# Optimization experiments

Measured on AMD Instinct MI355X. Metric: run time of the kernel, lower is better.

The kernel has to match this reference:

```python
import jax, jax.numpy as jnp
import numpy as np

EPS = 1e-5        # torch BatchNorm2d default eps
G = 8             # DCNv4 groups
KP = 9            # 3x3 kernel points


def conv2d(x, w):
    return jax.lax.conv_general_dilated(
        x, w, window_strides=(1, 1), padding='SAME',
        dimension_numbers=('NCHW', 'OIHW', 'NCHW'))


def bn_eval(x, g_, b_, m_, v_):
    s = g_ / jnp.sqrt(v_ + EPS)
    return x * s[None, :, None, None] + (b_ - m_ * s)[None, :, None, None]


def silu(x):
    return x * jax.nn.sigmoid(x)


def dcnv4_core(value, offset, mask):
    # value: (N,H,W,G,Cg)  offset: (N,H,W,G,K,2) (x,y)  mask: (N,H,W,G,K) unnormalized (DCNv4: no softmax)
    N, H, W, Gn, Cg = value.shape
    r = jnp.arange(-1, 2, dtype=value.dtype)              # dilation=1, pad=1, 3x3 grid
    gy, gx = jnp.meshgrid(r, r, indexing='ij')
    grid_x = gx.ravel()  # (9,)
    grid_y = gy.ravel()
    px = jnp.arange(W, dtype=value.dtype)[None, None, :, None, None] + grid_x + offset[..., 0]
    py = jnp.arange(H, dtype=value.dtype)[None, :, None, None, None] + grid_y + offset[..., 1]
    x0 = jnp.floor(px); y0 = jnp.floor(py)
    lx = px - x0; ly = py - y0
    x0i = x0.astype(jnp.int32); y0i = y0.astype(jnp.int32)
    bidx = jnp.arange(N)[:, None, None, None, None]
    gidx = jnp.arange(Gn)[None, None, None, :, None]

    def tap(yi, xi, wgt):
        valid = (yi >= 0) & (yi < H) & (xi >= 0) & (xi < W)   # zero padding outside
        v = value[bidx, jnp.clip(yi, 0, H - 1), jnp.clip(xi, 0, W - 1), gidx]  # (N,H,W,G,K,Cg)
        return v * (wgt * valid)[..., None]

    s = (tap(y0i, x0i, (1 - ly) * (1 - lx))
         + tap(y0i, x0i + 1, (1 - ly) * lx)
         + tap(y0i + 1, x0i, ly * (1 - lx))
         + tap(y0i + 1, x0i + 1, ly * lx))
    return jnp.einsum('nhwgkc,nhwgk->nhwgc', s, mask)


def dcnv4(x, val_w, val_b, om_w, om_b, outp_w, outp_b):
    # x: NCHW. DCNv4 wrapper: flatten to tokens, value_proj, offset_mask linear on raw tokens,
    # deformable aggregation, output_proj, back to NCHW.
    N, C, H, W = x.shape
    t = x.transpose(0, 2, 3, 1).reshape(N, H * W, C)
    value = (t @ val_w.T + val_b).reshape(N, H, W, G, C // G)
    om = (t @ om_w.T + om_b).reshape(N, H, W, G, KP * 3)  # per group: 2K offsets then K masks
    offset = om[..., :2 * KP].reshape(N, H, W, G, KP, 2)
    mask = om[..., 2 * KP:]
    out = dcnv4_core(value, offset, mask).reshape(N, H * W, C)
    out = out @ outp_w.T + outp_b
    return out.reshape(N, H, W, C).transpose(0, 3, 1, 2)


def setup_inputs() -> dict:
    key = jax.random.key(0)
    ks = jax.random.split(key, 32)
    W_SC = 0.05
    d = {}
    d['x'] = jax.random.normal(ks[0], (4, 256, 64, 64), jnp.float32)
    d['cv1_w'] = jax.random.normal(ks[1], (128, 256, 3, 3), jnp.float32) * W_SC
    d['cv1_bn_g'] = jax.random.uniform(ks[2], (128,), jnp.float32, 0.5, 1.5)
    d['cv1_bn_b'] = jax.random.normal(ks[3], (128,), jnp.float32) * 0.1
    d['cv1_bn_m'] = jax.random.normal(ks[4], (128,), jnp.float32) * 0.1
    d['cv1_bn_v'] = jax.random.uniform(ks[5], (128,), jnp.float32, 0.5, 1.5)
    d['cv2_w'] = jax.random.normal(ks[6], (256, 128, 3, 3), jnp.float32) * W_SC
    d['cv2_bn_g'] = jax.random.uniform(ks[7], (256,), jnp.float32, 0.5, 1.5)
    d['cv2_bn_b'] = jax.random.normal(ks[8], (256,), jnp.float32) * 0.1
    d['cv2_bn_m'] = jax.random.normal(ks[9], (256,), jnp.float32) * 0.1
    d['cv2_bn_v'] = jax.random.uniform(ks[10], (256,), jnp.float32, 0.5, 1.5)
    d['val_w'] = jax.random.normal(ks[11], (256, 256), jnp.float32) * W_SC
    d['val_b'] = jax.random.normal(ks[12], (256,), jnp.float32) * 0.01
    d['om_w'] = jax.random.normal(ks[13], (216, 256), jnp.float32) * 0.02
    d['om_b'] = jax.random.normal(ks[14], (216,), jnp.float32) * 0.01
    d['outp_w'] = jax.random.normal(ks[15], (256, 256), jnp.float32) * W_SC
    d['outp_b'] = jax.random.normal(ks[16], (256,), jnp.float32) * 0.01
    d['bn3_g'] = jax.random.uniform(ks[17], (256,), jnp.float32, 0.5, 1.5)
    d['bn3_b'] = jax.random.normal(ks[18], (256,), jnp.float32) * 0.1
    d['bn3_m'] = jax.random.normal(ks[19], (256,), jnp.float32) * 0.1
    d['bn3_v'] = jax.random.uniform(ks[20], (256,), jnp.float32, 0.5, 1.5)
    d['pw1_w'] = jax.random.normal(ks[21], (768, 256, 1, 1), jnp.float32) * W_SC
    d['pw1_b'] = jax.random.normal(ks[22], (768,), jnp.float32) * 0.01
    d['pw2_w'] = jax.random.normal(ks[23], (256, 768, 1, 1), jnp.float32) * W_SC
    d['pw2_b'] = jax.random.normal(ks[24], (256,), jnp.float32) * 0.01
    return d


def reference(x, cv1_w, cv1_bn_g, cv1_bn_b, cv1_bn_m, cv1_bn_v,
              cv2_w, cv2_bn_g, cv2_bn_b, cv2_bn_m, cv2_bn_v,
              val_w, val_b, om_w, om_b, outp_w, outp_b,
              bn3_g, bn3_b, bn3_m, bn3_v, pw1_w, pw1_b, pw2_w, pw2_b):
    # cv2(cv1(x)) branch: Conv = Conv2d(no bias) + BN + SiLU
    y = silu(bn_eval(conv2d(x, cv1_w), cv1_bn_g, cv1_bn_b, cv1_bn_m, cv1_bn_v))
    y = silu(bn_eval(conv2d(y, cv2_w), cv2_bn_g, cv2_bn_b, cv2_bn_m, cv2_bn_v))
    # dcn branch: DCNv4 -> BN -> 1x1 conv (+SiLU) -> 1x1 conv
    d = dcnv4(x, val_w, val_b, om_w, om_b, outp_w, outp_b)
    d = bn_eval(d, bn3_g, bn3_b, bn3_m, bn3_v)
    d = silu(conv2d(d, pw1_w) + pw1_b[None, :, None, None])
    d = conv2d(d, pw2_w) + pw2_b[None, :, None, None]
    return x + y + d
```

## Files before the change

### kernel.cpp

```cpp
#include <hip/hip_runtime.h>
#include <math.h>

typedef __attribute__((ext_vector_type(8))) __bf16 bf16x8;
typedef __attribute__((ext_vector_type(8))) unsigned short us8;
typedef __attribute__((ext_vector_type(4))) unsigned short us4;
typedef __attribute__((ext_vector_type(4))) float f32x4;
typedef __attribute__((ext_vector_type(4))) int i32x4;
typedef unsigned int uint32;

#define EPSV 1e-5f

__device__ __forceinline__ float silu_f(float v) { return v / (1.f + __expf(-v)); }

__device__ __forceinline__ unsigned short f2bf(float f) {
  uint32 u = __builtin_bit_cast(uint32, f);
  u += 0x7fffu + ((u >> 16) & 1u);
  return (unsigned short)(u >> 16);
}
__device__ __forceinline__ float bf2f(unsigned short h) {
  uint32 u = ((uint32)h) << 16;
  return __builtin_bit_cast(float, u);
}

__device__ __forceinline__ void gl_lds16(const void* g, void* l) {
  __builtin_amdgcn_global_load_lds(
      (const __attribute__((address_space(1))) unsigned int*)g,
      (__attribute__((address_space(3))) unsigned int*)l, 16, 0, 0);
}

template <int EPI, int CIN, int BN>
__device__ __forceinline__ void gemm_body(
    int rb, int cb, int k0, int KL,
    const unsigned short* __restrict__ A, const unsigned short* __restrict__ Bw,
    const float* __restrict__ bias, int K, int Co, void* __restrict__ outv,
    const float* __restrict__ e0, const float* __restrict__ e1,
    const float* __restrict__ e2, const float* __restrict__ e3,
    const unsigned short* __restrict__ zpage, bf16x8* smem) {
  constexpr int NFR = BN / 32;
  constexpr int NB = BN / 64;
  constexpr int CPB = 512 + BN * 4;
  const int t = threadIdx.x;
  const int lane = t & 63;
  const int wv = t >> 6;
  const int wr = wv >> 1, wc = wv & 1;

  f32x4 acc[4][NFR];
#pragma unroll
  for (int i = 0; i < 4; i++)
#pragma unroll
    for (int j = 0; j < NFR; j++) acc[i][j] = (f32x4){0.f, 0.f, 0.f, 0.f};

  const unsigned short* Abase[2];
  int aprow[2], apcol[2], akoff[2];
#pragma unroll
  for (int i = 0; i < 2; i++) {
    int c = t + 256 * i;
    int row = (c >> 6) * 16 + (c & 15);
    int koff = ((c >> 4) & 3) * 8;
    akoff[i] = koff;
    int grow = rb + row;
    if constexpr (CIN > 0) {
      int n = grow >> 12, p = grow & 4095;
      aprow[i] = p >> 6;
      apcol[i] = p & 63;
      Abase[i] = A + (size_t)n * 4096 * CIN;
    } else {
      Abase[i] = A + (size_t)grow * K + koff;
    }
  }
  const unsigned short* Bbase[NB];
#pragma unroll
  for (int i = 0; i < NB; i++) {
    int c = t + 256 * i;
    int col = cb + (c >> 6) * 16 + (c & 15);
    int koff = ((c >> 4) & 3) * 8;
    Bbase[i] = (col < Co) ? (Bw + (size_t)col * K + koff) : zpage;
  }
  auto addrA = [&](int i, int kb) -> const unsigned short* {
    if constexpr (CIN > 0) {
      int tap = kb / CIN;
      int ci = (kb & (CIN - 1)) + akoff[i];
      int dy = tap / 3 - 1, dx = tap % 3 - 1;
      int h = aprow[i] + dy, w = apcol[i] + dx;
      if (((unsigned)h < 64u) & ((unsigned)w < 64u))
        return &Abase[i][(size_t)(h * 64 + w) * CIN + ci];
      return zpage;
    } else {
      return Abase[i] + kb;
    }
  };
  auto stage = [&](int buf, int kb) {
    bf16x8* base = &smem[buf * CPB];
    gl_lds16(addrA(0, kb), (void*)&base[t]);
    gl_lds16(addrA(1, kb), (void*)&base[t + 256]);
    gl_lds16((Bbase[0] == zpage) ? zpage : Bbase[0] + kb, (void*)&base[512 + t]);
    if constexpr (NB == 2)
      gl_lds16((Bbase[1] == zpage) ? zpage : Bbase[1] + kb,
               (void*)&base[512 + t + 256]);
  };

  const int nt = KL >> 5;
  stage(0, k0);
  __syncthreads();
  int cur = 0;
  for (int it = 0; it < nt; ++it) {
    if (it + 1 < nt) stage(cur ^ 1, k0 + ((it + 1) << 5));
    const bf16x8* Ab = &smem[cur * CPB];
    const bf16x8* Bb = Ab + 512;
    bf16x8 af[4], bfr[NFR];
#pragma unroll
    for (int mi = 0; mi < 4; mi++) af[mi] = Ab[(wr * 4 + mi) * 64 + lane];
#pragma unroll
    for (int ni = 0; ni < NFR; ni++) bfr[ni] = Bb[(wc * NFR + ni) * 64 + lane];
    __builtin_amdgcn_s_setprio(1);
#pragma unroll
    for (int mi = 0; mi < 4; mi++)
#pragma unroll
      for (int ni = 0; ni < NFR; ni++)
        acc[mi][ni] = __builtin_amdgcn_mfma_f32_16x16x32_bf16(af[mi], bfr[ni],
                                                              acc[mi][ni], 0, 0, 0);
    __builtin_amdgcn_s_setprio(0);
    __syncthreads();
    cur ^= 1;
  }

  const int lr = lane & 15, kg4 = (lane >> 4) * 4;
#pragma unroll
  for (int mi = 0; mi < 4; mi++) {
#pragma unroll
    for (int ni = 0; ni < NFR; ni++) {
      int gcol = cb + wc * (BN / 2) + ni * 16 + lr;
      if (gcol >= Co) continue;
      float bval, s = 1.f, tt = 0.f;
      if (EPI == 2 || EPI == 7) bval = 0.f;
      else if (EPI == 5) bval = (gcol < 256) ? bias[gcol] : e0[gcol - 256];
      else bval = bias[gcol];
      if (EPI == 2 || EPI == 3) {
        s = e0[gcol] * rsqrtf(e3[gcol] + EPSV);
        tt = e1[gcol] - e2[gcol] * s;
      }
      if (EPI == 6) {
        int grow0 = rb + wr * 64 + mi * 16 + kg4;
        int n = grow0 >> 12, p0 = grow0 & 4095;
        size_t oix = ((size_t)(n * 256 + gcol)) * 4096 + p0;
        f32x4 xv = *(const f32x4*)&((const float*)e0)[oix];
        const unsigned short* y2p = (const unsigned short*)e1;
        f32x4 ov;
#pragma unroll
        for (int j = 0; j < 4; j++) {
          float y2 = bf2f(y2p[((size_t)(n * 4096 + p0 + j)) * 256 + gcol]);
          ov[j] = acc[mi][ni][j] + bval + xv[j] + y2;
        }
        *(f32x4*)&((float*)outv)[oix] = ov;
        continue;
      }
#pragma unroll
      for (int j = 0; j < 4; j++) {
        int grow = rb + wr * 64 + mi * 16 + kg4 + j;
        float v = acc[mi][ni][j] + bval;
        if (EPI == 2) v = silu_f(v * s + tt);
        if (EPI == 3) v = v * s + tt;
        if (EPI == 4) v = silu_f(v);
        if (EPI == 5) {
          if (gcol < 256)
            ((unsigned short*)outv)[(size_t)grow * 256 + gcol] = f2bf(v);
          else
            ((unsigned short*)e1)[(size_t)grow * 216 + (gcol - 256)] = f2bf(v);
        } else {
          ((unsigned short*)outv)[(size_t)grow * Co + gcol] = f2bf(v);
        }
      }
    }
  }
}

template <int EPI, int CIN>
__device__ __forceinline__ void gemm_body64(
    int rb, int cb, int k0, int KL,
    const unsigned short* __restrict__ A, const unsigned short* __restrict__ Bw,
    const float* __restrict__ bias, int K, int Co, void* __restrict__ outv,
    const float* __restrict__ e0, const float* __restrict__ e1,
    const float* __restrict__ e2, const float* __restrict__ e3,
    const unsigned short* __restrict__ zpage, bf16x8* smem) {
  constexpr int CPB = 1536;
  const int t = threadIdx.x;
  const int lane = t & 63;
  const int wv = t >> 6;
  const int wr = wv >> 1, wc = wv & 1;

  f32x4 acc[4][2];
#pragma unroll
  for (int i = 0; i < 4; i++)
#pragma unroll
    for (int j = 0; j < 2; j++) acc[i][j] = (f32x4){0.f, 0.f, 0.f, 0.f};

  const unsigned short* Abase[4];
  int aprow[4], apcol[4], akoff[4];
#pragma unroll
  for (int i = 0; i < 4; i++) {
    int c = t + 256 * i;
    int row = (c >> 7) * 16 + (c & 15);
    int koff = ((c >> 6) & 1) * 32 + ((c >> 4) & 3) * 8;
    akoff[i] = koff;
    int grow = rb + row;
    if constexpr (CIN > 0) {
      int n = grow >> 12, p = grow & 4095;
      aprow[i] = p >> 6;
      apcol[i] = p & 63;
      Abase[i] = A + (size_t)n * 4096 * CIN;
    } else {
      Abase[i] = A + (size_t)grow * K + koff;
    }
  }
  const unsigned short* Bbase[2];
#pragma unroll
  for (int i = 0; i < 2; i++) {
    int c = t + 256 * i;
    int col = cb + (c >> 7) * 16 + (c & 15);
    int koff = ((c >> 6) & 1) * 32 + ((c >> 4) & 3) * 8;
    Bbase[i] = (col < Co) ? (Bw + (size_t)col * K + koff) : zpage;
  }
  auto addrA = [&](int i, int kb) -> const unsigned short* {
    if constexpr (CIN > 0) {
      int tap = kb / CIN;
      int ci = (kb & (CIN - 1)) + akoff[i];
      int dy = tap / 3 - 1, dx = tap % 3 - 1;
      int h = aprow[i] + dy, w = apcol[i] + dx;
      if (((unsigned)h < 64u) & ((unsigned)w < 64u))
        return &Abase[i][(size_t)(h * 64 + w) * CIN + ci];
      return zpage;
    } else {
      return Abase[i] + kb;
    }
  };
  auto stage = [&](int buf, int kb) {
    bf16x8* base = &smem[buf * CPB];
#pragma unroll
    for (int i = 0; i < 4; i++)
      gl_lds16(addrA(i, kb), (void*)&base[t + 256 * i]);
    gl_lds16((Bbase[0] == zpage) ? zpage : Bbase[0] + kb,
             (void*)&base[1024 + t]);
    gl_lds16((Bbase[1] == zpage) ? zpage : Bbase[1] + kb,
             (void*)&base[1024 + t + 256]);
  };

  const int nt = KL >> 6;
  stage(0, k0);
  __syncthreads();
  int cur = 0;
  for (int it = 0; it < nt; ++it) {
    if (it + 1 < nt) stage(cur ^ 1, k0 + ((it + 1) << 6));
    const bf16x8* Ab = &smem[cur * CPB];
    const bf16x8* Bb = Ab + 1024;
    __builtin_amdgcn_s_setprio(1);
#pragma unroll
    for (int ks = 0; ks < 2; ks++) {
      bf16x8 af[4], bfr[2];
#pragma unroll
      for (int mi = 0; mi < 4; mi++)
        af[mi] = Ab[((wr * 4 + mi) * 2 + ks) * 64 + lane];
#pragma unroll
      for (int ni = 0; ni < 2; ni++)
        bfr[ni] = Bb[((wc * 2 + ni) * 2 + ks) * 64 + lane];
#pragma unroll
      for (int mi = 0; mi < 4; mi++)
#pragma unroll
        for (int ni = 0; ni < 2; ni++)
          acc[mi][ni] = __builtin_amdgcn_mfma_f32_16x16x32_bf16(
              af[mi], bfr[ni], acc[mi][ni], 0, 0, 0);
    }
    __builtin_amdgcn_s_setprio(0);
    __syncthreads();
    cur ^= 1;
  }

  const int lr = lane & 15, kg4 = (lane >> 4) * 4;
#pragma unroll
  for (int mi = 0; mi < 4; mi++) {
#pragma unroll
    for (int ni = 0; ni < 2; ni++) {
      int gcol = cb + wc * 32 + ni * 16 + lr;
      if (gcol >= Co) continue;
      float bval, s = 1.f, tt = 0.f;
      if (EPI == 2) bval = 0.f;
      else bval = bias[gcol];
      if (EPI == 2 || EPI == 3) {
        s = e0[gcol] * rsqrtf(e3[gcol] + EPSV);
        tt = e1[gcol] - e2[gcol] * s;
      }
      if (EPI == 6) {
        int grow0 = rb + wr * 64 + mi * 16 + kg4;
        int n = grow0 >> 12, p0 = grow0 & 4095;
        size_t oix = ((size_t)(n * 256 + gcol)) * 4096 + p0;
        f32x4 xv = *(const f32x4*)&((const float*)e0)[oix];
        const unsigned short* y2p = (const unsigned short*)e1;
        f32x4 ov;
#pragma unroll
        for (int j = 0; j < 4; j++) {
          float y2 = bf2f(y2p[((size_t)(n * 4096 + p0 + j)) * 256 + gcol]);
          ov[j] = acc[mi][ni][j] + bval + xv[j] + y2;
        }
        *(f32x4*)&((float*)outv)[oix] = ov;
        continue;
      }
#pragma unroll
      for (int j = 0; j < 4; j++) {
        int grow = rb + wr * 64 + mi * 16 + kg4 + j;
        float v = acc[mi][ni][j] + bval;
        if (EPI == 2) v = silu_f(v * s + tt);
        if (EPI == 3) v = v * s + tt;
        ((unsigned short*)outv)[(size_t)grow * Co + gcol] = f2bf(v);
      }
    }
  }
}

__device__ __forceinline__ void dcn_body(
    int bid, const unsigned short* __restrict__ value,
    const unsigned short* __restrict__ om, unsigned short* __restrict__ out,
    void* smemraw) {
  f32x4* wgt = (f32x4*)smemraw;
  i32x4* adr = (i32x4*)((char*)smemraw + 576 * 16);
  const int n = bid >> 9;
  const int p0 = (bid & 511) * 8;
  const int t = threadIdx.x;

  for (int idx = t; idx < 576; idx += 256) {
    int pi = idx / 72;
    int gk = idx - pi * 72;
    int g = gk / 9, k = gk - g * 9;
    int p = p0 + pi;
    int h0 = p >> 6, w0 = p & 63;
    const unsigned short* omp = om + ((size_t)(n * 4096 + p)) * 216 + g * 27;
    float ox = bf2f(omp[2 * k]), oy = bf2f(omp[2 * k + 1]);
    float mk = bf2f(omp[18 + k]);
    float px = (float)(w0 + (k % 3) - 1) + ox;
    float py = (float)(h0 + (k / 3) - 1) + oy;
    float x0f = floorf(px), y0f = floorf(py);
    float lx = px - x0f, ly = py - y0f;
    int x0 = (int)x0f, y0 = (int)y0f;
    int x1 = x0 + 1, y1 = y0 + 1;
    bool vx0 = (unsigned)x0 < 64u, vx1 = (unsigned)x1 < 64u;
    bool vy0 = (unsigned)y0 < 64u, vy1 = (unsigned)y1 < 64u;
    int cx0 = min(max(x0, 0), 63), cx1 = min(max(x1, 0), 63);
    int cy0 = min(max(y0, 0), 63), cy1 = min(max(y1, 0), 63);
    f32x4 w4;
    w4[0] = (1.f - ly) * (1.f - lx) * mk * (float)(vy0 && vx0);
    w4[1] = (1.f - ly) * lx * mk * (float)(vy0 && vx1);
    w4[2] = ly * (1.f - lx) * mk * (float)(vy1 && vx0);
    w4[3] = ly * lx * mk * (float)(vy1 && vx1);
    i32x4 a4;
    a4[0] = (cy0 * 64 + cx0) * 256;
    a4[1] = (cy0 * 64 + cx1) * 256;
    a4[2] = (cy1 * 64 + cx0) * 256;
    a4[3] = (cy1 * 64 + cx1) * 256;
    wgt[idx] = w4;
    adr[idx] = a4;
  }
  __syncthreads();

  const int pi = t >> 5;
  const int g = (t >> 2) & 7;
  const int l = t & 3;
  const int p = p0 + pi;
  const unsigned short* vb = value + ((size_t)n * 4096) * 256 + g * 32 + l * 8;
  const int bix = (pi * 8 + g) * 9;
  float a[8] = {0.f, 0.f, 0.f, 0.f, 0.f, 0.f, 0.f, 0.f};
#pragma unroll
  for (int k = 0; k < 9; k++) {
    f32x4 wv = wgt[bix + k];
    i32x4 av = adr[bix + k];
    us8 q0 = *(const us8*)(vb + av[0]);
    us8 q1 = *(const us8*)(vb + av[1]);
    us8 q2 = *(const us8*)(vb + av[2]);
    us8 q3 = *(const us8*)(vb + av[3]);
#pragma unroll
    for (int j = 0; j < 8; j++)
      a[j] += wv[0] * bf2f(q0[j]) + wv[1] * bf2f(q1[j]) +
              wv[2] * bf2f(q2[j]) + wv[3] * bf2f(q3[j]);
  }
  us8 o;
#pragma unroll
  for (int j = 0; j < 8; j++) o[j] = f2bf(a[j]);
  *(us8*)&out[((size_t)(n * 4096 + p)) * 256 + g * 32 + l * 8] = o;
}

__global__ __launch_bounds__(256) void prep_k(
    const float* __restrict__ x, unsigned short* __restrict__ xt,
    const float* __restrict__ c1, unsigned short* __restrict__ o1,
    const float* __restrict__ c2, unsigned short* __restrict__ o2,
    const float* __restrict__ a0, unsigned short* __restrict__ b0,
    const float* __restrict__ a1, unsigned short* __restrict__ b1,
    const float* __restrict__ a2, unsigned short* __restrict__ b2,
    const float* __restrict__ a3, unsigned short* __restrict__ b3,
    const float* __restrict__ a4, unsigned short* __restrict__ b4,
    uint32* __restrict__ zp) {
  __shared__ float lds[64][65];
  int b = blockIdx.x;
  const int t = threadIdx.x;
  if (b == 0 && t < 32) zp[t] = 0u;
  if (b < 1024) {
    const int p0 = (b & 63) * 64, c0 = ((b >> 6) & 3) * 64, n = b >> 8;
    const int pp = t & 63, ccb = t >> 6;
    const float* xb = x + ((size_t)n * 256 + c0) * 4096 + p0;
#pragma unroll
    for (int i = 0; i < 16; i++) {
      int cc = ccb * 16 + i;
      lds[pp][cc] = xb[(size_t)cc * 4096 + pp];
    }
    __syncthreads();
#pragma unroll
    for (int i = 0; i < 2; i++) {
      int pp2 = (t >> 3) + i * 32;
      int c8 = (t & 7) * 8;
      us8 v;
#pragma unroll
      for (int j = 0; j < 8; j++) v[j] = f2bf(lds[pp2][c8 + j]);
      *(us8*)&xt[((size_t)(n * 4096 + p0 + pp2)) * 256 + c0 + c8] = v;
    }
    return;
  }
  if (b < 1152) {
    int idx = (b - 1024) * 256 + t;
    int co = idx >> 8, ci = idx & 255;
    const float* src = c1 + (size_t)(co * 256 + ci) * 9;
#pragma unroll
    for (int tap = 0; tap < 9; tap++)
      o1[(size_t)(co * 9 + tap) * 256 + ci] = f2bf(src[tap]);
    return;
  }
  if (b < 1280) {
    int idx = (b - 1152) * 256 + t;
    int co = idx >> 7, ci = idx & 127;
    const float* src = c2 + (size_t)(co * 128 + ci) * 9;
#pragma unroll
    for (int tap = 0; tap < 9; tap++)
      o2[(size_t)(co * 9 + tap) * 128 + ci] = f2bf(src[tap]);
    return;
  }
  int idx = (b - 1280) * 256 + t;
  const float* s;
  unsigned short* d;
  int off;
  if (idx < 65536)       { s = a0; d = b0; off = idx; }
  else if (idx < 120832) { s = a1; d = b1; off = idx - 65536; }
  else if (idx < 186368) { s = a2; d = b2; off = idx - 120832; }
  else if (idx < 382976) { s = a3; d = b3; off = idx - 186368; }
  else if (idx < 579584) { s = a4; d = b4; off = idx - 382976; }
  else return;
  d[off] = f2bf(s[off]);
}

__global__ __launch_bounds__(256) void fused_s1(
    const unsigned short* __restrict__ xt,
    const unsigned short* __restrict__ wc1, unsigned short* __restrict__ part,
    const unsigned short* __restrict__ wval, const float* __restrict__ val_b,
    const float* __restrict__ om_b, unsigned short* __restrict__ omf,
    unsigned short* __restrict__ valt, const unsigned short* __restrict__ zpage) {
  __shared__ bf16x8 smem[2048];
  int b = blockIdx.x;
  if (b < 512) {
    int s = b >> 7, mt = b & 127;
    gemm_body<7, 256, 128>(mt * 128, 0, s * 576, 576, xt, wc1, nullptr, 2304,
                           128, part + (size_t)s * 2097152, nullptr, nullptr,
                           nullptr, nullptr, zpage, smem);
  } else {
    b -= 512;
    gemm_body<5, 0, 128>((b >> 2) * 128, (b & 3) * 128, 0, 256, xt, wval, val_b,
                         256, 472, valt, om_b, (const float*)(const void*)omf,
                         nullptr, nullptr, zpage, smem);
  }
}

__global__ __launch_bounds__(256) void fused_r(
    const unsigned short* __restrict__ part, const float* __restrict__ g1,
    const float* __restrict__ bb1, const float* __restrict__ m1,
    const float* __restrict__ v1, unsigned short* __restrict__ y1t,
    const unsigned short* __restrict__ valt, const unsigned short* __restrict__ omf,
    unsigned short* __restrict__ dcnt) {
  __shared__ char rsm[18432];
  int b = blockIdx.x;
  if (b < 1024) {
    int g = b * 256 + threadIdx.x;
    int grow = g >> 4;
    int co8 = (g & 15) << 3;
    size_t base = (size_t)grow * 128 + co8;
    float sum[8] = {0.f, 0.f, 0.f, 0.f, 0.f, 0.f, 0.f, 0.f};
#pragma unroll
    for (int s = 0; s < 4; s++) {
      us8 pv = *(const us8*)&part[base + (size_t)s * 2097152];
#pragma unroll
      for (int j = 0; j < 8; j++) sum[j] += bf2f(pv[j]);
    }
    us8 o;
#pragma unroll
    for (int j = 0; j < 8; j++) {
      int co = co8 + j;
      float sc = g1[co] * rsqrtf(v1[co] + EPSV);
      float tt = bb1[co] - m1[co] * sc;
      o[j] = f2bf(silu_f(sum[j] * sc + tt));
    }
    *(us8*)&y1t[base] = o;
  } else {
    dcn_body(b - 1024, valt, omf, dcnt, (void*)rsm);
  }
}

__global__ __launch_bounds__(256) void fused_s2(
    const unsigned short* __restrict__ y1t,
    const unsigned short* __restrict__ wc2, const float* __restrict__ g2,
    const float* __restrict__ bb2, const float* __restrict__ m2,
    const float* __restrict__ v2, unsigned short* __restrict__ y2t,
    const unsigned short* __restrict__ dcnt, const unsigned short* __restrict__ woutp,
    const float* __restrict__ outp_b, const float* __restrict__ g3,
    const float* __restrict__ bb3, const float* __restrict__ m3,
    const float* __restrict__ v3, unsigned short* __restrict__ d1t,
    const unsigned short* __restrict__ zpage) {
  __shared__ bf16x8 smem[3072];
  int b = blockIdx.x;
  if (b < 512) {
    gemm_body64<2, 128>((b >> 2) * 128, (b & 3) * 64, 0, 1152, y1t, wc2,
                        nullptr, 1152, 256, y2t, g2, bb2, m2, v2, zpage, smem);
  } else {
    b -= 512;
    gemm_body64<3, 0>((b >> 2) * 128, (b & 3) * 64, 0, 256, dcnt, woutp,
                      outp_b, 256, 256, d1t, g3, bb3, m3, v3, zpage, smem);
  }
}

template <int EPI, int CIN, int BN>
__global__ __launch_bounds__(256) void gemm_k(
    const unsigned short* __restrict__ A, const unsigned short* __restrict__ Bw,
    const float* __restrict__ bias, int K, int Co, void* __restrict__ outv,
    const float* __restrict__ e0, const float* __restrict__ e1,
    const float* __restrict__ e2, const float* __restrict__ e3,
    const unsigned short* __restrict__ zpage) {
  __shared__ bf16x8 smem[2 * (512 + BN * 4)];
  gemm_body<EPI, CIN, BN>(blockIdx.y * 128, blockIdx.x * BN, 0, K, A, Bw, bias,
                          K, Co, outv, e0, e1, e2, e3, zpage, smem);
}

template <int EPI>
__global__ __launch_bounds__(256) void gemm_k64(
    const unsigned short* __restrict__ A, const unsigned short* __restrict__ Bw,
    const float* __restrict__ bias, int K, int Co, void* __restrict__ outv,
    const float* __restrict__ e0, const float* __restrict__ e1,
    const float* __restrict__ e2, const float* __restrict__ e3,
    const unsigned short* __restrict__ zpage) {
  __shared__ bf16x8 smem[3072];
  gemm_body64<EPI, 0>(blockIdx.y * 128, blockIdx.x * 64, 0, K, A, Bw, bias,
                      K, Co, outv, e0, e1, e2, e3, zpage, smem);
}

extern "C" void kernel_launch(void* const* d_in, const int* in_sizes, int n_in,
                              void* d_out, int out_size, void* d_ws,
                              size_t ws_size, hipStream_t stream) {
  const float* x      = (const float*)d_in[0];
  const float* cv1_w  = (const float*)d_in[1];
  const float* cv1_g  = (const float*)d_in[2];
  const float* cv1_b  = (const float*)d_in[3];
  const float* cv1_m  = (const float*)d_in[4];
  const float* cv1_v  = (const float*)d_in[5];
  const float* cv2_w  = (const float*)d_in[6];
  const float* cv2_g  = (const float*)d_in[7];
  const float* cv2_b  = (const float*)d_in[8];
  const float* cv2_m  = (const float*)d_in[9];
  const float* cv2_v  = (const float*)d_in[10];
  const float* val_w  = (const float*)d_in[11];
  const float* val_b  = (const float*)d_in[12];
  const float* om_w   = (const float*)d_in[13];
  const float* om_b   = (const float*)d_in[14];
  const float* outp_w = (const float*)d_in[15];
  const float* outp_b = (const float*)d_in[16];
  const float* bn3_g  = (const float*)d_in[17];
  const float* bn3_b  = (const float*)d_in[18];
  const float* bn3_m  = (const float*)d_in[19];
  const float* bn3_v  = (const float*)d_in[20];
  const float* pw1_w  = (const float*)d_in[21];
  const float* pw1_b  = (const float*)d_in[22];
  const float* pw2_w  = (const float*)d_in[23];
  const float* pw2_b  = (const float*)d_in[24];
  float* out = (float*)d_out;

  char* w = (char*)d_ws;
  auto alloc = [&](size_t bytes) {
    char* p = w;
    w += (bytes + 255) & ~(size_t)255;
    return p;
  };
  unsigned short* xt    = (unsigned short*)alloc(16384ull * 256 * 2);
  unsigned short* y1t   = (unsigned short*)alloc(16384ull * 128 * 2);
  unsigned short* y2t   = (unsigned short*)alloc(16384ull * 256 * 2);
  unsigned short* valt  = (unsigned short*)alloc(16384ull * 256 * 2);
  unsigned short* omf   = (unsigned short*)alloc(16384ull * 216 * 2);
  unsigned short* dcnt  = (unsigned short*)alloc(16384ull * 256 * 2);
  unsigned short* d1t   = (unsigned short*)alloc(16384ull * 256 * 2);
  unsigned short* p1t   = (unsigned short*)alloc(16384ull * 768 * 2);
  unsigned short* part = d1t;
  unsigned short* wc1   = (unsigned short*)alloc(128ull * 2304 * 2);
  unsigned short* wc2   = (unsigned short*)alloc(256ull * 1152 * 2);
  unsigned short* wval  = (unsigned short*)alloc(256ull * 256 * 2);
  unsigned short* wom   = (unsigned short*)alloc(216ull * 256 * 2);
  unsigned short* woutp = (unsigned short*)alloc(256ull * 256 * 2);
  unsigned short* wpw1  = (unsigned short*)alloc(768ull * 256 * 2);
  unsigned short* wpw2  = (unsigned short*)alloc(256ull * 768 * 2);
  unsigned short* zpage = (unsigned short*)alloc(256);

  prep_k<<<3544, 256, 0, stream>>>(x, xt, cv1_w, wc1, cv2_w, wc2, val_w, wval,
                                   om_w, wom, outp_w, woutp, pw1_w, wpw1,
                                   pw2_w, wpw2, (uint32*)zpage);

  fused_s1<<<1024, 256, 0, stream>>>(xt, wc1, part, wval, val_b, om_b, omf,
                                     valt, zpage);

  fused_r<<<3072, 256, 0, stream>>>(part, cv1_g, cv1_b, cv1_m, cv1_v, y1t,
                                    valt, omf, dcnt);

  fused_s2<<<1024, 256, 0, stream>>>(y1t, wc2, cv2_g, cv2_b, cv2_m, cv2_v, y2t,
                                     dcnt, woutp, outp_b, bn3_g, bn3_b, bn3_m,
                                     bn3_v, d1t, zpage);

  gemm_k<4, 0, 128><<<dim3(6, 128), 256, 0, stream>>>(
      d1t, wpw1, pw1_b, 256, 768, p1t, nullptr, nullptr, nullptr, nullptr, zpage);
  gemm_k64<6><<<dim3(4, 128), 256, 0, stream>>>(
      p1t, wpw2, pw2_b, 768, 256, out, x, (const float*)y2t, nullptr, nullptr, zpage);
}
```

Measured before the change: 156.0 us.

## Rebalance kernel stages: move weight casts into s1, pair cv2 with pw1

Weight conversion for cv2, outp, pw1 and pw2 moves out of the prep kernel into extra blocks of the first fused GEMM kernel. The ones that only do elementwise casts are vectorised four wide. The cv2 3x3 GEMM now shares a launch with the pw1 GEMM instead of the outp GEMM, and outp runs alone first. The aim is to shorten the serial prep stage and balance work across launches by pairing independent GEMMs. The launch count stays the same, but the cv2 GEMM now runs one stage later, next to pw1, and the kernels mix blocks of different shapes.

```diff
diff --git a/kernel.cpp b/kernel.cpp
--- a/kernel.cpp
+++ b/kernel.cpp
@@ -388,12 +388,8 @@
 __global__ __launch_bounds__(256) void prep_k(
     const float* __restrict__ x, unsigned short* __restrict__ xt,
     const float* __restrict__ c1, unsigned short* __restrict__ o1,
-    const float* __restrict__ c2, unsigned short* __restrict__ o2,
     const float* __restrict__ a0, unsigned short* __restrict__ b0,
     const float* __restrict__ a1, unsigned short* __restrict__ b1,
-    const float* __restrict__ a2, unsigned short* __restrict__ b2,
-    const float* __restrict__ a3, unsigned short* __restrict__ b3,
-    const float* __restrict__ a4, unsigned short* __restrict__ b4,
     uint32* __restrict__ zp) {
   __shared__ float lds[64][65];
   int b = blockIdx.x;
@@ -429,26 +425,9 @@
       o1[(size_t)(co * 9 + tap) * 256 + ci] = f2bf(src[tap]);
     return;
   }
-  if (b < 1280) {
-    int idx = (b - 1152) * 256 + t;
-    int co = idx >> 7, ci = idx & 127;
-    const float* src = c2 + (size_t)(co * 128 + ci) * 9;
-#pragma unroll
-    for (int tap = 0; tap < 9; tap++)
-      o2[(size_t)(co * 9 + tap) * 128 + ci] = f2bf(src[tap]);
-    return;
-  }
-  int idx = (b - 1280) * 256 + t;
-  const float* s;
-  unsigned short* d;
-  int off;
-  if (idx < 65536)       { s = a0; d = b0; off = idx; }
-  else if (idx < 120832) { s = a1; d = b1; off = idx - 65536; }
-  else if (idx < 186368) { s = a2; d = b2; off = idx - 120832; }
-  else if (idx < 382976) { s = a3; d = b3; off = idx - 186368; }
-  else if (idx < 579584) { s = a4; d = b4; off = idx - 382976; }
-  else return;
-  d[off] = f2bf(s[off]);
+  int idx = (b - 1152) * 256 + t;
+  if (idx < 65536) b0[idx] = f2bf(a0[idx]);
+  else if (idx < 120832) b1[idx - 65536] = f2bf(a1[idx - 65536]);
 }
 
 __global__ __launch_bounds__(256) void fused_s1(
@@ -456,19 +435,44 @@
     const unsigned short* __restrict__ wc1, unsigned short* __restrict__ part,
     const unsigned short* __restrict__ wval, const float* __restrict__ val_b,
     const float* __restrict__ om_b, unsigned short* __restrict__ omf,
-    unsigned short* __restrict__ valt, const unsigned short* __restrict__ zpage) {
+    unsigned short* __restrict__ valt, const unsigned short* __restrict__ zpage,
+    const float* __restrict__ outp_w, unsigned short* __restrict__ woutp,
+    const float* __restrict__ pw1_w, unsigned short* __restrict__ wpw1,
+    const float* __restrict__ pw2_w, unsigned short* __restrict__ wpw2,
+    const float* __restrict__ cv2_w, unsigned short* __restrict__ wc2) {
   __shared__ bf16x8 smem[2048];
   int b = blockIdx.x;
+  const int t = threadIdx.x;
   if (b < 512) {
     int s = b >> 7, mt = b & 127;
     gemm_body<7, 256, 128>(mt * 128, 0, s * 576, 576, xt, wc1, nullptr, 2304,
                            128, part + (size_t)s * 2097152, nullptr, nullptr,
                            nullptr, nullptr, zpage, smem);
-  } else {
-    b -= 512;
-    gemm_body<5, 0, 128>((b >> 2) * 128, (b & 3) * 128, 0, 256, xt, wval, val_b,
+  } else if (b < 1024) {
+    int v = b - 512;
+    gemm_body<5, 0, 128>((v >> 2) * 128, (v & 3) * 128, 0, 256, xt, wval, val_b,
                          256, 472, valt, om_b, (const float*)(const void*)omf,
                          nullptr, nullptr, zpage, smem);
+  } else if (b < 1472) {
+    int idx4 = (b - 1024) * 1024 + t * 4;
+    const float* s;
+    unsigned short* d;
+    int off;
+    if (idx4 < 65536)       { s = outp_w; d = woutp; off = idx4; }
+    else if (idx4 < 262144) { s = pw1_w;  d = wpw1;  off = idx4 - 65536; }
+    else                    { s = pw2_w;  d = wpw2;  off = idx4 - 262144; }
+    f32x4 v = *(const f32x4*)&s[off];
+    us4 o;
+#pragma unroll
+    for (int j = 0; j < 4; j++) o[j] = f2bf(v[j]);
+    *(us4*)&d[off] = o;
+  } else {
+    int idx = (b - 1472) * 256 + t;
+    int co = idx >> 7, ci = idx & 127;
+    const float* src = cv2_w + (size_t)(co * 128 + ci) * 9;
+#pragma unroll
+    for (int tap = 0; tap < 9; tap++)
+      wc2[(size_t)(co * 9 + tap) * 128 + ci] = f2bf(src[tap]);
   }
 }
 
@@ -506,11 +510,7 @@
   }
 }
 
-__global__ __launch_bounds__(256) void fused_s2(
-    const unsigned short* __restrict__ y1t,
-    const unsigned short* __restrict__ wc2, const float* __restrict__ g2,
-    const float* __restrict__ bb2, const float* __restrict__ m2,
-    const float* __restrict__ v2, unsigned short* __restrict__ y2t,
+__global__ __launch_bounds__(256) void s2_outp(
     const unsigned short* __restrict__ dcnt, const unsigned short* __restrict__ woutp,
     const float* __restrict__ outp_b, const float* __restrict__ g3,
     const float* __restrict__ bb3, const float* __restrict__ m3,
@@ -518,38 +518,41 @@
     const unsigned short* __restrict__ zpage) {
   __shared__ bf16x8 smem[3072];
   int b = blockIdx.x;
+  gemm_body64<3, 0>((b >> 2) * 128, (b & 3) * 64, 0, 256, dcnt, woutp,
+                    outp_b, 256, 256, d1t, g3, bb3, m3, v3, zpage, smem);
+}
+
+__global__ __launch_bounds__(256) void fused_p(
+    const unsigned short* __restrict__ y1t,
+    const unsigned short* __restrict__ wc2, const float* __restrict__ g2,
+    const float* __restrict__ bb2, const float* __restrict__ m2,
+    const float* __restrict__ v2, unsigned short* __restrict__ y2t,
+    const unsigned short* __restrict__ d1t, const unsigned short* __restrict__ wpw1,
+    const float* __restrict__ pw1_b, unsigned short* __restrict__ p1t,
+    const unsigned short* __restrict__ zpage) {
+  __shared__ bf16x8 smem[3072];
+  int b = blockIdx.x;
   if (b < 512) {
     gemm_body64<2, 128>((b >> 2) * 128, (b & 3) * 64, 0, 1152, y1t, wc2,
                         nullptr, 1152, 256, y2t, g2, bb2, m2, v2, zpage, smem);
   } else {
-    b -= 512;
-    gemm_body64<3, 0>((b >> 2) * 128, (b & 3) * 64, 0, 256, dcnt, woutp,
-                      outp_b, 256, 256, d1t, g3, bb3, m3, v3, zpage, smem);
-  }
-}
-
-template <int EPI, int CIN, int BN>
-__global__ __launch_bounds__(256) void gemm_k(
-    const unsigned short* __restrict__ A, const unsigned short* __restrict__ Bw,
-    const float* __restrict__ bias, int K, int Co, void* __restrict__ outv,
-    const float* __restrict__ e0, const float* __restrict__ e1,
-    const float* __restrict__ e2, const float* __restrict__ e3,
-    const unsigned short* __restrict__ zpage) {
-  __shared__ bf16x8 smem[2 * (512 + BN * 4)];
-  gemm_body<EPI, CIN, BN>(blockIdx.y * 128, blockIdx.x * BN, 0, K, A, Bw, bias,
-                          K, Co, outv, e0, e1, e2, e3, zpage, smem);
-}
-
-template <int EPI>
-__global__ __launch_bounds__(256) void gemm_k64(
-    const unsigned short* __restrict__ A, const unsigned short* __restrict__ Bw,
-    const float* __restrict__ bias, int K, int Co, void* __restrict__ outv,
-    const float* __restrict__ e0, const float* __restrict__ e1,
-    const float* __restrict__ e2, const float* __restrict__ e3,
+    int q = b - 512;
+    gemm_body<4, 0, 128>((q / 6) * 128, (q % 6) * 128, 0, 256, d1t, wpw1,
+                         pw1_b, 256, 768, p1t, nullptr, nullptr, nullptr,
+                         nullptr, zpage, smem);
+  }
+}
+
+__global__ __launch_bounds__(256) void pw2_k(
+    const unsigned short* __restrict__ p1t, const unsigned short* __restrict__ wpw2,
+    const float* __restrict__ pw2_b, const float* __restrict__ x,
+    const unsigned short* __restrict__ y2t, float* __restrict__ out,
     const unsigned short* __restrict__ zpage) {
   __shared__ bf16x8 smem[3072];
-  gemm_body64<EPI, 0>(blockIdx.y * 128, blockIdx.x * 64, 0, K, A, Bw, bias,
-                      K, Co, outv, e0, e1, e2, e3, zpage, smem);
+  int b = blockIdx.x;
+  gemm_body64<6, 0>((b >> 2) * 128, (b & 3) * 64, 0, 768, p1t, wpw2, pw2_b,
+                    768, 256, out, x, (const float*)(const void*)y2t,
+                    nullptr, nullptr, zpage, smem);
 }
 
 extern "C" void kernel_launch(void* const* d_in, const int* in_sizes, int n_in,
@@ -606,22 +609,21 @@
   unsigned short* wpw2  = (unsigned short*)alloc(256ull * 768 * 2);
   unsigned short* zpage = (unsigned short*)alloc(256);
 
-  prep_k<<<3544, 256, 0, stream>>>(x, xt, cv1_w, wc1, cv2_w, wc2, val_w, wval,
-                                   om_w, wom, outp_w, woutp, pw1_w, wpw1,
-                                   pw2_w, wpw2, (uint32*)zpage);
-
-  fused_s1<<<1024, 256, 0, stream>>>(xt, wc1, part, wval, val_b, om_b, omf,
-                                     valt, zpage);
+  prep_k<<<1624, 256, 0, stream>>>(x, xt, cv1_w, wc1, val_w, wval, om_w, wom,
+                                   (uint32*)zpage);
+
+  fused_s1<<<1600, 256, 0, stream>>>(xt, wc1, part, wval, val_b, om_b, omf,
+                                     valt, zpage, outp_w, woutp, pw1_w, wpw1,
+                                     pw2_w, wpw2, cv2_w, wc2);
 
   fused_r<<<3072, 256, 0, stream>>>(part, cv1_g, cv1_b, cv1_m, cv1_v, y1t,
                                     valt, omf, dcnt);
 
-  fused_s2<<<1024, 256, 0, stream>>>(y1t, wc2, cv2_g, cv2_b, cv2_m, cv2_v, y2t,
-                                     dcnt, woutp, outp_b, bn3_g, bn3_b, bn3_m,
-                                     bn3_v, d1t, zpage);
-
-  gemm_k<4, 0, 128><<<dim3(6, 128), 256, 0, stream>>>(
-      d1t, wpw1, pw1_b, 256, 768, p1t, nullptr, nullptr, nullptr, nullptr, zpage);
-  gemm_k64<6><<<dim3(4, 128), 256, 0, stream>>>(
-      p1t, wpw2, pw2_b, 768, 256, out, x, (const float*)y2t, nullptr, nullptr, zpage);
-}
+  s2_outp<<<512, 256, 0, stream>>>(dcnt, woutp, outp_b, bn3_g, bn3_b, bn3_m,
+                                   bn3_v, d1t, zpage);
+
+  fused_p<<<1280, 256, 0, stream>>>(y1t, wc2, cv2_g, cv2_b, cv2_m, cv2_v, y2t,
+                                    d1t, wpw1, pw1_b, p1t, zpage);
+
+  pw2_k<<<512, 256, 0, stream>>>(p1t, wpw2, pw2_b, x, y2t, out, zpage);
+}
```

After: 152.9 us. 2.0% less time.
